# Performance work log

Hardware: AMD Instinct MI355X
Metric: run time of the kernel (lower is better)

## Reference

```python
import jax, jax.numpy as jnp
import numpy as np

B_, S_, D_, N_, R_ = 2, 2048, 1024, 16, 64  # batch, seq, d_model, d_state, dt_rank


def setup_inputs() -> dict:
    key = jax.random.key(0)
    ks = jax.random.split(key, 12)
    x = jax.random.normal(ks[0], (B_, S_, D_), dtype=jnp.float32)
    # params (xavier-ish scale)
    W_dtw = jax.random.normal(ks[1], (R_, D_), dtype=jnp.float32) * (1.0 / np.sqrt(D_))
    W_dt = jax.random.normal(ks[2], (D_, R_), dtype=jnp.float32) * (1.0 / np.sqrt(R_))
    b_dt = jnp.zeros((D_,), dtype=jnp.float32)
    A_log = jnp.log(jax.random.uniform(ks[3], (D_, N_), minval=0.5, maxval=1.5, dtype=jnp.float32))
    W_B = jax.random.normal(ks[4], (N_, D_), dtype=jnp.float32) * (1.0 / np.sqrt(D_))
    W_C = jax.random.normal(ks[5], (N_, D_), dtype=jnp.float32) * (1.0 / np.sqrt(D_))
    Dp = jnp.ones((D_,), dtype=jnp.float32)
    ln_g = jnp.ones((D_,), dtype=jnp.float32)
    ln_b = jnp.zeros((D_,), dtype=jnp.float32)
    W_out = jax.random.normal(ks[6], (D_, D_), dtype=jnp.float32) * (1.0 / np.sqrt(D_))
    return {"x": x, "W_dtw": W_dtw, "W_dt": W_dt, "b_dt": b_dt, "A_log": A_log,
            "W_B": W_B, "W_C": W_C, "Dp": Dp, "ln_g": ln_g, "ln_b": ln_b, "W_out": W_out}


def _layernorm(y, g, b, eps=1e-5):
    mu = jnp.mean(y, axis=-1, keepdims=True)
    var = jnp.mean(jnp.square(y - mu), axis=-1, keepdims=True)
    return (y - mu) * jax.lax.rsqrt(var + eps) * g + b


def reference(x, W_dtw, W_dt, b_dt, A_log, W_B, W_C, Dp, ln_g, ln_b, W_out):
    # projections
    dt = jnp.einsum('bsd,rd->bsr', x, W_dtw)                 # [B,S,R]
    delta = jax.nn.softplus(jnp.einsum('bsr,dr->bsd', dt, W_dt) + b_dt)  # [B,S,D]
    Bm = jnp.einsum('bsd,nd->bsn', x, W_B)                   # [B,S,N]
    Cm = jnp.einsum('bsd,nd->bsn', x, W_C)                   # [B,S,N]
    A = -jnp.exp(A_log)                                      # [D,N]

    def step(h, inp):
        d_t, b_t, c_t, x_t = inp                             # [B,D],[B,N],[B,N],[B,D]
        dA = jnp.exp(d_t[..., None] * A)                     # [B,D,N]
        h = dA * h + (d_t[..., None] * b_t[:, None, :]) * x_t[..., None]
        y_t = jnp.sum(h * c_t[:, None, :], axis=-1)          # [B,D]
        return h, y_t

    h0 = jnp.zeros((x.shape[0], x.shape[2], A.shape[1]), dtype=x.dtype)
    xs = (jnp.swapaxes(delta, 0, 1), jnp.swapaxes(Bm, 0, 1),
          jnp.swapaxes(Cm, 0, 1), jnp.swapaxes(x, 0, 1))
    _, ys = jax.lax.scan(step, h0, xs)                       # ys: [S,B,D]
    y = jnp.swapaxes(ys, 0, 1) + Dp * x                      # [B,S,D]
    y = _layernorm(y, ln_g, ln_b)
    return jnp.einsum('bsd,ed->bse', y, W_out)
```

## Files before the change

kernel.cpp:

```cpp
#include <hip/hip_runtime.h>
#include <hip/hip_bf16.h>

#define B_ 2
#define S_ 2048
#define D_ 1024
#define N_ 16
#define R_ 64
#define NC 64
#define CL 32
#define BS_ (B_*S_)

typedef __attribute__((ext_vector_type(4))) float f32x4;
typedef __attribute__((ext_vector_type(8))) short bf16x8;
typedef __attribute__((ext_vector_type(8))) unsigned short u16x8;

__device__ __forceinline__ unsigned short f2b(float v) {
  unsigned u = __builtin_bit_cast(unsigned, v);
  unsigned r = ((u >> 16) & 1u) + 0x7FFFu;
  return (unsigned short)((u + r) >> 16);
}

__device__ __forceinline__ void gload_lds16(const void* g, void* l) {
  __builtin_amdgcn_global_load_lds(
      (const __attribute__((address_space(1))) unsigned int*)g,
      (__attribute__((address_space(3))) unsigned int*)l, 16, 0, 0);
}

__global__ __launch_bounds__(256) void k_castall(
    const float* __restrict__ x, const float* __restrict__ W_B,
    const float* __restrict__ W_C, const float* __restrict__ W_dt,
    const float* __restrict__ W_out, const float* __restrict__ W_dtw,
    unsigned short* __restrict__ xb, unsigned short* __restrict__ WBC,
    unsigned short* __restrict__ wdtb, unsigned short* __restrict__ wob,
    unsigned short* __restrict__ wdtwT) {
  int i = (blockIdx.x * 256 + threadIdx.x) * 4;
  if (i < 5341184) {
    const float* s; unsigned short* d; int off;
    if (i < 4194304)      { s = x;     d = xb;          off = 0; }
    else if (i < 4210688) { s = W_B;   d = WBC;         off = 4194304; }
    else if (i < 4227072) { s = W_C;   d = WBC + 16384; off = 4210688; }
    else if (i < 4292608) { s = W_dt;  d = wdtb;        off = 4227072; }
    else                  { s = W_out; d = wob;         off = 4292608; }
    int j = i - off;
    float4 v = *(const float4*)&s[j];
    ushort4 o;
    o.x = f2b(v.x); o.y = f2b(v.y); o.z = f2b(v.z); o.w = f2b(v.w);
    *(ushort4*)&d[j] = o;
  } else {
    int j = i - 5341184;
    int r = j >> 10, e = j & 1023;
    float4 v = *(const float4*)&W_dtw[j];
    wdtwT[(size_t)(e + 0) * 64 + r] = f2b(v.x);
    wdtwT[(size_t)(e + 1) * 64 + r] = f2b(v.y);
    wdtwT[(size_t)(e + 2) * 64 + r] = f2b(v.z);
    wdtwT[(size_t)(e + 3) * 64 + r] = f2b(v.w);
  }
}

__global__ __launch_bounds__(256) void k_weff(
    const unsigned short* __restrict__ wdtb, const unsigned short* __restrict__ wdtwT,
    unsigned short* __restrict__ weff) {
  __shared__ __align__(16) unsigned short As[128 * 64];
  __shared__ __align__(16) unsigned short Bs[128 * 64];
  const int tid = threadIdx.x;
  const int lane = tid & 63, wid = tid >> 6;
  const int wr = wid >> 1, wc = wid & 1;
  const size_t row0 = (size_t)blockIdx.x * 128;
  const size_t col0 = (size_t)blockIdx.y * 128;
  f32x4 acc[4][4] = {};
  {
    const int r = tid >> 3, s = tid & 7;
    #pragma unroll
    for (int i = 0; i < 4; ++i) {
      const int row = i * 32 + r;
      const int gs = s ^ (row & 7);
      gload_lds16(wdtb + (row0 + row) * R_ + gs * 8, As + row * 64 + s * 8);
      gload_lds16(wdtwT + (col0 + row) * R_ + gs * 8, Bs + row * 64 + s * 8);
    }
  }
  __syncthreads();
  const int r = lane & 15, kg = lane >> 4;
  #pragma unroll
  for (int ks = 0; ks < 2; ++ks) {
    bf16x8 a[4], b[4];
    #pragma unroll
    for (int m = 0; m < 4; ++m) {
      const int arow = wr * 64 + m * 16 + r;
      a[m] = *(const bf16x8*)&As[arow * 64 + (((ks << 2) | kg) ^ (arow & 7)) * 8];
    }
    #pragma unroll
    for (int n = 0; n < 4; ++n) {
      const int brow = wc * 64 + n * 16 + r;
      b[n] = *(const bf16x8*)&Bs[brow * 64 + (((ks << 2) | kg) ^ (brow & 7)) * 8];
    }
    #pragma unroll
    for (int m = 0; m < 4; ++m)
      #pragma unroll
      for (int n = 0; n < 4; ++n)
        acc[m][n] = __builtin_amdgcn_mfma_f32_16x16x32_bf16(a[m], b[n], acc[m][n], 0, 0, 0);
  }
  const int cr = lane >> 4, cc = lane & 15;
  #pragma unroll
  for (int m = 0; m < 4; ++m)
    #pragma unroll
    for (int n = 0; n < 4; ++n)
      #pragma unroll
      for (int j = 0; j < 4; ++j)
        weff[(row0 + wr * 64 + m * 16 + cr * 4 + j) * D_ + col0 + wc * 64 + n * 16 + cc]
            = f2b(acc[m][n][j]);
}

__device__ __forceinline__ void stage64x64(const unsigned short* __restrict__ g,
                                           size_t row0, int k0,
                                           unsigned short* lds, int tid) {
  const int r = tid >> 3, s = tid & 7;
  #pragma unroll
  for (int i = 0; i < 2; ++i) {
    const int row = i * 32 + r;
    const int gs = s ^ (row & 7);
    gload_lds16(g + ((row0 + row) << 10) + k0 + (gs << 3), lds + row * 64 + s * 8);
  }
}

__global__ __launch_bounds__(256, 4) void k_deltaBC(
    const unsigned short* __restrict__ xb, const unsigned short* __restrict__ weff,
    const unsigned short* __restrict__ WBC, const float* __restrict__ b_dt,
    float* __restrict__ delta, float* __restrict__ Bm, float* __restrict__ Cm) {
  __shared__ __align__(16) unsigned short As[2][64 * 64];
  __shared__ __align__(16) unsigned short Bs[2][64 * 64];
  const int tid = threadIdx.x;
  const int lane = tid & 63, wid = tid >> 6;
  const size_t row0 = (size_t)blockIdx.x * 64;
  const int by = blockIdx.y;
  const bool bc = (by == 16);
  f32x4 acc[4] = {};

  auto stageB = [&](int buf, int k0) {
    if (!bc) {
      stage64x64(weff, (size_t)by * 64, k0, Bs[buf], tid);
    } else {
      const int row = tid >> 3, s = tid & 7;
      const int gs = s ^ (row & 7);
      gload_lds16(WBC + (size_t)row * D_ + k0 + (gs << 3), Bs[buf] + row * 64 + s * 8);
    }
  };

  stage64x64(xb, row0, 0, As[0], tid);
  stageB(0, 0);
  __syncthreads();

  int cur = 0;
  const int r = lane & 15, kg = lane >> 4;
  for (int t = 0; t < 16; ++t) {
    if (t + 1 < 16) {
      stage64x64(xb, row0, (t + 1) * 64, As[cur ^ 1], tid);
      stageB(cur ^ 1, (t + 1) * 64);
    }
    if (!bc) {
      #pragma unroll
      for (int ks = 0; ks < 2; ++ks) {
        const int arow = wid * 16 + r;
        bf16x8 a = *(const bf16x8*)&As[cur][arow * 64 + (((ks << 2) | kg) ^ (arow & 7)) * 8];
        bf16x8 b0, b1, b2, b3;
        b0 = *(const bf16x8*)&Bs[cur][(0 * 16 + r) * 64 + (((ks << 2) | kg) ^ ((0 * 16 + r) & 7)) * 8];
        b1 = *(const bf16x8*)&Bs[cur][(1 * 16 + r) * 64 + (((ks << 2) | kg) ^ ((1 * 16 + r) & 7)) * 8];
        b2 = *(const bf16x8*)&Bs[cur][(2 * 16 + r) * 64 + (((ks << 2) | kg) ^ ((2 * 16 + r) & 7)) * 8];
        b3 = *(const bf16x8*)&Bs[cur][(3 * 16 + r) * 64 + (((ks << 2) | kg) ^ ((3 * 16 + r) & 7)) * 8];
        acc[0] = __builtin_amdgcn_mfma_f32_16x16x32_bf16(a, b0, acc[0], 0, 0, 0);
        acc[1] = __builtin_amdgcn_mfma_f32_16x16x32_bf16(a, b1, acc[1], 0, 0, 0);
        acc[2] = __builtin_amdgcn_mfma_f32_16x16x32_bf16(a, b2, acc[2], 0, 0, 0);
        acc[3] = __builtin_amdgcn_mfma_f32_16x16x32_bf16(a, b3, acc[3], 0, 0, 0);
      }
    } else {
      #pragma unroll
      for (int ks = 0; ks < 2; ++ks) {
        const int arow = wid * 16 + r;
        bf16x8 a = *(const bf16x8*)&As[cur][arow * 64 + (((ks << 2) | kg) ^ (arow & 7)) * 8];
        bf16x8 b0, b1;
        b0 = *(const bf16x8*)&Bs[cur][(0 * 16 + r) * 64 + (((ks << 2) | kg) ^ ((0 * 16 + r) & 7)) * 8];
        b1 = *(const bf16x8*)&Bs[cur][(1 * 16 + r) * 64 + (((ks << 2) | kg) ^ ((1 * 16 + r) & 7)) * 8];
        acc[0] = __builtin_amdgcn_mfma_f32_16x16x32_bf16(a, b0, acc[0], 0, 0, 0);
        acc[1] = __builtin_amdgcn_mfma_f32_16x16x32_bf16(a, b1, acc[1], 0, 0, 0);
      }
    }
    __syncthreads();
    cur ^= 1;
  }

  const int cr = lane >> 4, cc = lane & 15;
  if (!bc) {
    #pragma unroll
    for (int n = 0; n < 4; ++n) {
      const int d = by * 64 + n * 16 + cc;
      const float bd = b_dt[d];
      #pragma unroll
      for (int j = 0; j < 4; ++j) {
        size_t trow = row0 + wid * 16 + cr * 4 + j;
        float v = acc[n][j] + bd;
        float sp = fmaxf(v, 0.f) + log1pf(__expf(-fabsf(v)));
        delta[trow * D_ + d] = sp;
      }
    }
  } else {
    #pragma unroll
    for (int n = 0; n < 2; ++n) {
      const int col = n * 16 + cc;
      #pragma unroll
      for (int j = 0; j < 4; ++j) {
        size_t trow = row0 + wid * 16 + cr * 4 + j;
        float v = acc[n][j];
        if (col < 16) Bm[trow * N_ + col] = v;
        else          Cm[trow * N_ + col - 16] = v;
      }
    }
  }
}

__global__ __launch_bounds__(256) void k_scan1(
    const float* __restrict__ x, const float* __restrict__ delta,
    const float* __restrict__ Bm, const float* __restrict__ A_log,
    float* __restrict__ sdsum, float* __restrict__ hend) {
  __shared__ __align__(16) float sd[CL][64];
  __shared__ __align__(16) float sx[CL][64];
  __shared__ __align__(16) float sB[CL][N_];
  const int tid = threadIdx.x;
  const int db = blockIdx.x & 15;
  const int c  = (blockIdx.x >> 4) & (NC - 1);
  const int b  = blockIdx.x >> 10;
  const int d0 = db * 64;
  const size_t tokbase = (size_t)(b * S_ + c * CL);

  {
    int s = tid >> 4, jf = (tid & 15) * 4;
    size_t g = (tokbase + s) * D_ + d0 + jf;
    gload_lds16(&delta[g], &sd[s][jf]);
    gload_lds16(&x[g],     &sx[s][jf]);
    gload_lds16(&delta[g + (size_t)16 * D_], &sd[s + 16][jf]);
    gload_lds16(&x[g + (size_t)16 * D_],     &sx[s + 16][jf]);
    if (tid < 128) {
      int s2 = tid >> 2, nf = (tid & 3) * 4;
      gload_lds16(&Bm[(tokbase + s2) * N_ + nf], &sB[s2][nf]);
    }
  }
  const int nq = tid & 3, dl = tid >> 2;
  const int d = d0 + dl;
  float4 av = *(const float4*)&A_log[(size_t)d * N_ + nq * 4];
  float Ad0 = -__expf(av.x), Ad1 = -__expf(av.y);
  float Ad2 = -__expf(av.z), Ad3 = -__expf(av.w);
  __syncthreads();

  float sds = 0.f;
  float h0 = 0.f, h1 = 0.f, h2 = 0.f, h3 = 0.f;
  #pragma unroll 8
  for (int s = 0; s < CL; ++s) {
    float dlt = sd[s][dl];
    float dbx = dlt * sx[s][dl];
    sds += dlt;
    float4 Bv = *(const float4*)&sB[s][nq * 4];
    float da0 = __expf(dlt * Ad0), da1 = __expf(dlt * Ad1);
    float da2 = __expf(dlt * Ad2), da3 = __expf(dlt * Ad3);
    h0 = da0 * h0 + dbx * Bv.x;
    h1 = da1 * h1 + dbx * Bv.y;
    h2 = da2 * h2 + dbx * Bv.z;
    h3 = da3 * h3 + dbx * Bv.w;
  }
  size_t o = (((size_t)(b * NC + c)) * D_ + d) * N_ + nq * 4;
  *(float4*)&hend[o] = make_float4(h0, h1, h2, h3);
  if (nq == 0) sdsum[(size_t)(b * NC + c) * D_ + d] = sds;
}

__global__ __launch_bounds__(256) void k_scan2(
    const float* __restrict__ sdsum, const float* __restrict__ hend,
    const float* __restrict__ A_log, float* __restrict__ hstart) {
  const int tid = threadIdx.x;
  const int o  = tid & 7;
  const int n  = (tid >> 3) & 15;
  const int dl = tid >> 7;
  const int d2 = blockIdx.x & 511;
  const int b  = blockIdx.x >> 9;
  const int d  = d2 * 2 + dl;
  const float Ad = -__expf(A_log[(size_t)d * N_ + n]);

  float ap8[8], he8[8];
  float A_loc = 1.f, H_loc = 0.f;
  #pragma unroll
  for (int k = 0; k < 8; ++k) {
    const int c = o * 8 + k;
    float sds = sdsum[(size_t)(b * NC + c) * D_ + d];
    float ap = __expf(Ad * sds);
    float he = hend[((size_t)(b * NC + c) * D_ + d) * N_ + n];
    ap8[k] = ap; he8[k] = he;
    A_loc *= ap;
    H_loc = ap * H_loc + he;
  }
  float h = 0.f;
  const int gb = (tid & 63) & ~7;
  #pragma unroll
  for (int j = 0; j < 7; ++j) {
    float Aj = __shfl(A_loc, gb | j, 64);
    float Hj = __shfl(H_loc, gb | j, 64);
    if (o > j) h = Aj * h + Hj;
  }
  #pragma unroll
  for (int k = 0; k < 8; ++k) {
    const int c = o * 8 + k;
    hstart[((size_t)(b * NC + c) * D_ + d) * N_ + n] = h;
    h = ap8[k] * h + he8[k];
  }
}

__global__ __launch_bounds__(256) void k_scan3(
    const float* __restrict__ x, const float* __restrict__ delta,
    const float* __restrict__ Bm, const float* __restrict__ Cm,
    const float* __restrict__ A_log, const float* __restrict__ hstart,
    const float* __restrict__ Dp, float* __restrict__ ypre) {
  __shared__ __align__(16) float sd[CL][64];
  __shared__ __align__(16) float sx[CL][64];
  __shared__ __align__(16) float sB[CL][N_];
  __shared__ __align__(16) float sC[CL][N_];
  __shared__ __align__(16) float sy[CL][64];
  const int tid = threadIdx.x;
  const int db = blockIdx.x & 15;
  const int c  = (blockIdx.x >> 4) & (NC - 1);
  const int b  = blockIdx.x >> 10;
  const int d0 = db * 64;
  const size_t tokbase = (size_t)(b * S_ + c * CL);

  {
    int s = tid >> 4, jf = (tid & 15) * 4;
    size_t g = (tokbase + s) * D_ + d0 + jf;
    gload_lds16(&delta[g], &sd[s][jf]);
    gload_lds16(&x[g],     &sx[s][jf]);
    gload_lds16(&delta[g + (size_t)16 * D_], &sd[s + 16][jf]);
    gload_lds16(&x[g + (size_t)16 * D_],     &sx[s + 16][jf]);
    if (tid < 128) {
      int s2 = tid >> 2, nf = (tid & 3) * 4;
      gload_lds16(&Bm[(tokbase + s2) * N_ + nf], &sB[s2][nf]);
      gload_lds16(&Cm[(tokbase + s2) * N_ + nf], &sC[s2][nf]);
    }
  }
  const int nq = tid & 3, dl = tid >> 2;
  const int d = d0 + dl;
  float4 av = *(const float4*)&A_log[(size_t)d * N_ + nq * 4];
  float Ad0 = -__expf(av.x), Ad1 = -__expf(av.y);
  float Ad2 = -__expf(av.z), Ad3 = -__expf(av.w);
  float h0, h1, h2, h3;
  {
    size_t o = (((size_t)(b * NC + c)) * D_ + d) * N_ + nq * 4;
    float4 v = *(const float4*)&hstart[o];
    h0 = v.x; h1 = v.y; h2 = v.z; h3 = v.w;
  }
  const float Dpd = Dp[d];
  __syncthreads();

  #pragma unroll 8
  for (int s = 0; s < CL; ++s) {
    float dlt = sd[s][dl];
    float xv  = sx[s][dl];
    float dbx = dlt * xv;
    float4 Bv = *(const float4*)&sB[s][nq * 4];
    float4 Cv = *(const float4*)&sC[s][nq * 4];
    float da0 = __expf(dlt * Ad0), da1 = __expf(dlt * Ad1);
    float da2 = __expf(dlt * Ad2), da3 = __expf(dlt * Ad3);
    h0 = da0 * h0 + dbx * Bv.x;
    h1 = da1 * h1 + dbx * Bv.y;
    h2 = da2 * h2 + dbx * Bv.z;
    h3 = da3 * h3 + dbx * Bv.w;
    float y = h0 * Cv.x + h1 * Cv.y + h2 * Cv.z + h3 * Cv.w;
    y += __shfl_xor(y, 1);
    y += __shfl_xor(y, 2);
    if (nq == 0) sy[s][dl] = y + Dpd * xv;
  }
  __syncthreads();
  {
    int s = tid >> 3, j = (tid & 7) * 8;
    size_t g = (tokbase + s) * D_ + d0 + j;
    *(float4*)&ypre[g]     = *(float4*)&sy[s][j];
    *(float4*)&ypre[g + 4] = *(float4*)&sy[s][j + 4];
  }
}

__device__ __forceinline__ float block_sum256(float v, float* sm) {
  #pragma unroll
  for (int o = 32; o > 0; o >>= 1) v += __shfl_down(v, o, 64);
  int w = threadIdx.x >> 6;
  __syncthreads();
  if ((threadIdx.x & 63) == 0) sm[w] = v;
  __syncthreads();
  return (sm[0] + sm[1]) + (sm[2] + sm[3]);
}

__global__ __launch_bounds__(256) void k_ln(
    const float* __restrict__ ypre, const float* __restrict__ g,
    const float* __restrict__ bta, unsigned short* __restrict__ ybf) {
  __shared__ float sm[4];
  const int t = blockIdx.x;
  const int tid = threadIdx.x;
  size_t base = (size_t)t * D_ + tid * 4;
  float4 v = *(const float4*)&ypre[base];
  float s1 = block_sum256(v.x + v.y + v.z + v.w, sm);
  float mu = s1 * (1.f / D_);
  float cx = v.x - mu, cy = v.y - mu, cz = v.z - mu, cw = v.w - mu;
  float s2 = block_sum256(cx*cx + cy*cy + cz*cz + cw*cw, sm);
  float rs = rsqrtf(s2 * (1.f / D_) + 1e-5f);
  float4 gg = *(const float4*)&g[tid * 4];
  float4 bb = *(const float4*)&bta[tid * 4];
  ushort4 o;
  o.x = f2b(cx * rs * gg.x + bb.x);
  o.y = f2b(cy * rs * gg.y + bb.y);
  o.z = f2b(cz * rs * gg.z + bb.z);
  o.w = f2b(cw * rs * gg.w + bb.w);
  *(ushort4*)&ybf[base] = o;
}

__global__ __launch_bounds__(256, 4) void k_out(const unsigned short* __restrict__ Y,
                                                const unsigned short* __restrict__ W,
                                                float* __restrict__ O) {
  __shared__ __align__(16) unsigned short As[2][64 * 64];
  __shared__ __align__(16) unsigned short Bs[2][64 * 64];
  const int tid = threadIdx.x;
  const int lane = tid & 63, wid = tid >> 6;
  const size_t row0 = (size_t)blockIdx.x * 64;
  const size_t col0 = (size_t)blockIdx.y * 64;
  f32x4 acc[4] = {};

  stage64x64(Y, row0, 0, As[0], tid);
  stage64x64(W, col0, 0, Bs[0], tid);
  __syncthreads();

  int cur = 0;
  const int r = lane & 15, kg = lane >> 4;
  for (int t = 0; t < 16; ++t) {
    if (t + 1 < 16) {
      stage64x64(Y, row0, (t + 1) * 64, As[cur ^ 1], tid);
      stage64x64(W, col0, (t + 1) * 64, Bs[cur ^ 1], tid);
    }
    #pragma unroll
    for (int ks = 0; ks < 2; ++ks) {
      const int arow = wid * 16 + r;
      bf16x8 a = *(const bf16x8*)&As[cur][arow * 64 + (((ks << 2) | kg) ^ (arow & 7)) * 8];
      bf16x8 b0, b1, b2, b3;
      b0 = *(const bf16x8*)&Bs[cur][(0 * 16 + r) * 64 + (((ks << 2) | kg) ^ ((0 * 16 + r) & 7)) * 8];
      b1 = *(const bf16x8*)&Bs[cur][(1 * 16 + r) * 64 + (((ks << 2) | kg) ^ ((1 * 16 + r) & 7)) * 8];
      b2 = *(const bf16x8*)&Bs[cur][(2 * 16 + r) * 64 + (((ks << 2) | kg) ^ ((2 * 16 + r) & 7)) * 8];
      b3 = *(const bf16x8*)&Bs[cur][(3 * 16 + r) * 64 + (((ks << 2) | kg) ^ ((3 * 16 + r) & 7)) * 8];
      acc[0] = __builtin_amdgcn_mfma_f32_16x16x32_bf16(a, b0, acc[0], 0, 0, 0);
      acc[1] = __builtin_amdgcn_mfma_f32_16x16x32_bf16(a, b1, acc[1], 0, 0, 0);
      acc[2] = __builtin_amdgcn_mfma_f32_16x16x32_bf16(a, b2, acc[2], 0, 0, 0);
      acc[3] = __builtin_amdgcn_mfma_f32_16x16x32_bf16(a, b3, acc[3], 0, 0, 0);
    }
    __syncthreads();
    cur ^= 1;
  }

  const int cr = lane >> 4, cc = lane & 15;
  #pragma unroll
  for (int n = 0; n < 4; ++n) {
    size_t orow = row0 + wid * 16 + cr * 4;
    float* op = O + orow * D_ + col0 + n * 16 + cc;
    #pragma unroll
    for (int j = 0; j < 4; ++j) op[(size_t)j * D_] = acc[n][j];
  }
}

extern "C" void kernel_launch(void* const* d_in, const int* in_sizes, int n_in,
                              void* d_out, int out_size, void* d_ws, size_t ws_size,
                              hipStream_t stream) {
  const float* x     = (const float*)d_in[0];
  const float* W_dtw = (const float*)d_in[1];
  const float* W_dt  = (const float*)d_in[2];
  const float* b_dt  = (const float*)d_in[3];
  const float* A_log = (const float*)d_in[4];
  const float* W_B   = (const float*)d_in[5];
  const float* W_C   = (const float*)d_in[6];
  const float* Dp    = (const float*)d_in[7];
  const float* ln_g  = (const float*)d_in[8];
  const float* ln_b  = (const float*)d_in[9];
  const float* W_out = (const float*)d_in[10];
  float* out = (float*)d_out;

  float* ws = (float*)d_ws;
  float* delta  = ws;
  float* ypre   = delta  + (size_t)BS_ * D_;
  float* Bm     = ypre   + (size_t)BS_ * D_;
  float* Cm     = Bm     + (size_t)BS_ * N_;
  float* hend   = Cm     + (size_t)BS_ * N_;
  float* hstart = hend   + (size_t)B_ * NC * D_ * N_;
  float* sdsum  = hstart + (size_t)B_ * NC * D_ * N_;
  unsigned short* xb    = (unsigned short*)(sdsum + (size_t)B_ * NC * D_);
  unsigned short* WBC   = xb    + (size_t)BS_ * D_;
  unsigned short* wdtb  = WBC   + (size_t)32 * D_;
  unsigned short* wdtwT = wdtb  + (size_t)D_ * R_;
  unsigned short* weff  = wdtwT + (size_t)D_ * R_;
  unsigned short* wob   = weff  + (size_t)D_ * D_;
  unsigned short* ybf   = wob   + (size_t)D_ * D_;

  k_castall<<<dim3(5280), dim3(256), 0, stream>>>(x, W_B, W_C, W_dt, W_out, W_dtw,
                                                  xb, WBC, wdtb, wob, wdtwT);
  k_weff<<<dim3(8, 8), dim3(256), 0, stream>>>(wdtb, wdtwT, weff);
  k_deltaBC<<<dim3(BS_ / 64, 17), dim3(256), 0, stream>>>(xb, weff, WBC, b_dt,
                                                          delta, Bm, Cm);
  k_scan1<<<dim3(B_ * NC * (D_ / 64)), dim3(256), 0, stream>>>(x, delta, Bm, A_log,
                                                               sdsum, hend);
  k_scan2<<<dim3(B_ * (D_ / 2)), dim3(256), 0, stream>>>(sdsum, hend, A_log, hstart);
  k_scan3<<<dim3(B_ * NC * (D_ / 64)), dim3(256), 0, stream>>>(x, delta, Bm, Cm,
                                                               A_log, hstart, Dp, ypre);
  k_ln<<<dim3(BS_), dim3(256), 0, stream>>>(ypre, ln_g, ln_b, ybf);
  k_out<<<dim3(BS_ / 64, D_ / 64), dim3(256), 0, stream>>>(ybf, wob, out);
}
```

Measured before the change: 115.8 us.

## Fuse chunked scan phases into one cooperative kernel and fold weff cast

Merges the three scan kernels into a single cooperative kernel with two grid-wide syncs. Each block handles two chunks and computes the local zero-start scan output once, then adds the carry-in correction hstart·C·exp(A·cumdelta) afterwards, so delta and x are no longer reloaded in a second full scan. The separate W_dtw transpose, cast and MFMA weff kernels are replaced by a simple FP32 dot-product path inside the cast kernel, which removes one launch. In exchange it pays for grid-sync overhead, reads B and C straight from global memory instead of LDS, and requires all 1024 blocks to be co-resident.

```diff
diff --git a/kernel.cpp b/kernel.cpp
--- a/kernel.cpp
+++ b/kernel.cpp
@@ -1,5 +1,8 @@
 #include <hip/hip_runtime.h>
 #include <hip/hip_bf16.h>
+#include <hip/hip_cooperative_groups.h>
+
+namespace cg = cooperative_groups;
 
 #define B_ 2
 #define S_ 2048
@@ -26,88 +29,39 @@
       (__attribute__((address_space(3))) unsigned int*)l, 16, 0, 0);
 }
 
-__global__ __launch_bounds__(256) void k_castall(
+__global__ __launch_bounds__(256) void k_castweff(
     const float* __restrict__ x, const float* __restrict__ W_B,
-    const float* __restrict__ W_C, const float* __restrict__ W_dt,
-    const float* __restrict__ W_out, const float* __restrict__ W_dtw,
+    const float* __restrict__ W_C, const float* __restrict__ W_out,
+    const float* __restrict__ W_dt, const float* __restrict__ W_dtw,
     unsigned short* __restrict__ xb, unsigned short* __restrict__ WBC,
-    unsigned short* __restrict__ wdtb, unsigned short* __restrict__ wob,
-    unsigned short* __restrict__ wdtwT) {
-  int i = (blockIdx.x * 256 + threadIdx.x) * 4;
-  if (i < 5341184) {
-    const float* s; unsigned short* d; int off;
-    if (i < 4194304)      { s = x;     d = xb;          off = 0; }
-    else if (i < 4210688) { s = W_B;   d = WBC;         off = 4194304; }
-    else if (i < 4227072) { s = W_C;   d = WBC + 16384; off = 4210688; }
-    else if (i < 4292608) { s = W_dt;  d = wdtb;        off = 4227072; }
-    else                  { s = W_out; d = wob;         off = 4292608; }
-    int j = i - off;
+    unsigned short* __restrict__ wob, unsigned short* __restrict__ weff) {
+  const int blk = blockIdx.x, tid = threadIdx.x;
+  if (blk < 5152) {
+    const float* s; unsigned short* d; int base;
+    if (blk < 4096)      { s = x;     d = xb;          base = 0; }
+    else if (blk < 4112) { s = W_B;   d = WBC;         base = 4096; }
+    else if (blk < 4128) { s = W_C;   d = WBC + 16384; base = 4112; }
+    else                 { s = W_out; d = wob;         base = 4128; }
+    int j = (blk - base) * 1024 + tid * 4;
     float4 v = *(const float4*)&s[j];
     ushort4 o;
     o.x = f2b(v.x); o.y = f2b(v.y); o.z = f2b(v.z); o.w = f2b(v.w);
     *(ushort4*)&d[j] = o;
   } else {
-    int j = i - 5341184;
-    int r = j >> 10, e = j & 1023;
-    float4 v = *(const float4*)&W_dtw[j];
-    wdtwT[(size_t)(e + 0) * 64 + r] = f2b(v.x);
-    wdtwT[(size_t)(e + 1) * 64 + r] = f2b(v.y);
-    wdtwT[(size_t)(e + 2) * 64 + r] = f2b(v.z);
-    wdtwT[(size_t)(e + 3) * 64 + r] = f2b(v.w);
-  }
-}
-
-__global__ __launch_bounds__(256) void k_weff(
-    const unsigned short* __restrict__ wdtb, const unsigned short* __restrict__ wdtwT,
-    unsigned short* __restrict__ weff) {
-  __shared__ __align__(16) unsigned short As[128 * 64];
-  __shared__ __align__(16) unsigned short Bs[128 * 64];
-  const int tid = threadIdx.x;
-  const int lane = tid & 63, wid = tid >> 6;
-  const int wr = wid >> 1, wc = wid & 1;
-  const size_t row0 = (size_t)blockIdx.x * 128;
-  const size_t col0 = (size_t)blockIdx.y * 128;
-  f32x4 acc[4][4] = {};
-  {
-    const int r = tid >> 3, s = tid & 7;
-    #pragma unroll
-    for (int i = 0; i < 4; ++i) {
-      const int row = i * 32 + r;
-      const int gs = s ^ (row & 7);
-      gload_lds16(wdtb + (row0 + row) * R_ + gs * 8, As + row * 64 + s * 8);
-      gload_lds16(wdtwT + (col0 + row) * R_ + gs * 8, Bs + row * 64 + s * 8);
-    }
-  }
-  __syncthreads();
-  const int r = lane & 15, kg = lane >> 4;
-  #pragma unroll
-  for (int ks = 0; ks < 2; ++ks) {
-    bf16x8 a[4], b[4];
-    #pragma unroll
-    for (int m = 0; m < 4; ++m) {
-      const int arow = wr * 64 + m * 16 + r;
-      a[m] = *(const bf16x8*)&As[arow * 64 + (((ks << 2) | kg) ^ (arow & 7)) * 8];
-    }
-    #pragma unroll
-    for (int n = 0; n < 4; ++n) {
-      const int brow = wc * 64 + n * 16 + r;
-      b[n] = *(const bf16x8*)&Bs[brow * 64 + (((ks << 2) | kg) ^ (brow & 7)) * 8];
-    }
-    #pragma unroll
-    for (int m = 0; m < 4; ++m)
-      #pragma unroll
-      for (int n = 0; n < 4; ++n)
-        acc[m][n] = __builtin_amdgcn_mfma_f32_16x16x32_bf16(a[m], b[n], acc[m][n], 0, 0, 0);
-  }
-  const int cr = lane >> 4, cc = lane & 15;
-  #pragma unroll
-  for (int m = 0; m < 4; ++m)
-    #pragma unroll
-    for (int n = 0; n < 4; ++n)
-      #pragma unroll
-      for (int j = 0; j < 4; ++j)
-        weff[(row0 + wr * 64 + m * 16 + cr * 4 + j) * D_ + col0 + wc * 64 + n * 16 + cc]
-            = f2b(acc[m][n][j]);
+    const int dd = blk - 5152;
+    const float* wdt = W_dt + (size_t)dd * R_;
+    const int e4 = tid * 4;
+    float a0 = 0.f, a1 = 0.f, a2 = 0.f, a3 = 0.f;
+    #pragma unroll 8
+    for (int r = 0; r < R_; ++r) {
+      float w = wdt[r];
+      float4 ww = *(const float4*)&W_dtw[(size_t)r * D_ + e4];
+      a0 += w * ww.x; a1 += w * ww.y; a2 += w * ww.z; a3 += w * ww.w;
+    }
+    ushort4 o;
+    o.x = f2b(a0); o.y = f2b(a1); o.z = f2b(a2); o.w = f2b(a3);
+    *(ushort4*)&weff[(size_t)dd * D_ + e4] = o;
+  }
 }
 
 __device__ __forceinline__ void stage64x64(const unsigned short* __restrict__ g,
@@ -216,30 +170,31 @@
   }
 }
 
-__global__ __launch_bounds__(256) void k_scan1(
+__global__ __launch_bounds__(256, 4) void k_scanall(
     const float* __restrict__ x, const float* __restrict__ delta,
-    const float* __restrict__ Bm, const float* __restrict__ A_log,
-    float* __restrict__ sdsum, float* __restrict__ hend) {
-  __shared__ __align__(16) float sd[CL][64];
-  __shared__ __align__(16) float sx[CL][64];
-  __shared__ __align__(16) float sB[CL][N_];
+    const float* __restrict__ Bm, const float* __restrict__ Cm,
+    const float* __restrict__ A_log, const float* __restrict__ Dp,
+    float* __restrict__ sdsum, float* __restrict__ hend,
+    float* __restrict__ hstart, float* __restrict__ ypre) {
+  __shared__ __align__(16) float sd[2][CL][64];
+  __shared__ __align__(16) float sx[2][CL][64];
   const int tid = threadIdx.x;
-  const int db = blockIdx.x & 15;
-  const int c  = (blockIdx.x >> 4) & (NC - 1);
-  const int b  = blockIdx.x >> 10;
-  const int d0 = db * 64;
-  const size_t tokbase = (size_t)(b * S_ + c * CL);
+  const int slab = blockIdx.x & 15;
+  const int cp   = (blockIdx.x >> 4) & 31;
+  const int b    = blockIdx.x >> 9;
+  const int d0 = slab * 64;
+  const int c0 = cp * 2;
 
   {
     int s = tid >> 4, jf = (tid & 15) * 4;
-    size_t g = (tokbase + s) * D_ + d0 + jf;
-    gload_lds16(&delta[g], &sd[s][jf]);
-    gload_lds16(&x[g],     &sx[s][jf]);
-    gload_lds16(&delta[g + (size_t)16 * D_], &sd[s + 16][jf]);
-    gload_lds16(&x[g + (size_t)16 * D_],     &sx[s + 16][jf]);
-    if (tid < 128) {
-      int s2 = tid >> 2, nf = (tid & 3) * 4;
-      gload_lds16(&Bm[(tokbase + s2) * N_ + nf], &sB[s2][nf]);
+    #pragma unroll
+    for (int cc = 0; cc < 2; ++cc) {
+      size_t tokb = (size_t)(b * S_ + (c0 + cc) * CL);
+      size_t g = (tokb + s) * D_ + d0 + jf;
+      gload_lds16(&delta[g],                   &sd[cc][s][jf]);
+      gload_lds16(&delta[g + (size_t)16 * D_], &sd[cc][s + 16][jf]);
+      gload_lds16(&x[g],                       &sx[cc][s][jf]);
+      gload_lds16(&x[g + (size_t)16 * D_],     &sx[cc][s + 16][jf]);
     }
   }
   const int nq = tid & 3, dl = tid >> 2;
@@ -247,136 +202,106 @@
   float4 av = *(const float4*)&A_log[(size_t)d * N_ + nq * 4];
   float Ad0 = -__expf(av.x), Ad1 = -__expf(av.y);
   float Ad2 = -__expf(av.z), Ad3 = -__expf(av.w);
-  __syncthreads();
-
-  float sds = 0.f;
-  float h0 = 0.f, h1 = 0.f, h2 = 0.f, h3 = 0.f;
-  #pragma unroll 8
-  for (int s = 0; s < CL; ++s) {
-    float dlt = sd[s][dl];
-    float dbx = dlt * sx[s][dl];
-    sds += dlt;
-    float4 Bv = *(const float4*)&sB[s][nq * 4];
-    float da0 = __expf(dlt * Ad0), da1 = __expf(dlt * Ad1);
-    float da2 = __expf(dlt * Ad2), da3 = __expf(dlt * Ad3);
-    h0 = da0 * h0 + dbx * Bv.x;
-    h1 = da1 * h1 + dbx * Bv.y;
-    h2 = da2 * h2 + dbx * Bv.z;
-    h3 = da3 * h3 + dbx * Bv.w;
-  }
-  size_t o = (((size_t)(b * NC + c)) * D_ + d) * N_ + nq * 4;
-  *(float4*)&hend[o] = make_float4(h0, h1, h2, h3);
-  if (nq == 0) sdsum[(size_t)(b * NC + c) * D_ + d] = sds;
-}
-
-__global__ __launch_bounds__(256) void k_scan2(
-    const float* __restrict__ sdsum, const float* __restrict__ hend,
-    const float* __restrict__ A_log, float* __restrict__ hstart) {
-  const int tid = threadIdx.x;
-  const int o  = tid & 7;
-  const int n  = (tid >> 3) & 15;
-  const int dl = tid >> 7;
-  const int d2 = blockIdx.x & 511;
-  const int b  = blockIdx.x >> 9;
-  const int d  = d2 * 2 + dl;
-  const float Ad = -__expf(A_log[(size_t)d * N_ + n]);
-
-  float ap8[8], he8[8];
-  float A_loc = 1.f, H_loc = 0.f;
+  const float Dpd = Dp[d];
+  __syncthreads();
+
   #pragma unroll
-  for (int k = 0; k < 8; ++k) {
-    const int c = o * 8 + k;
-    float sds = sdsum[(size_t)(b * NC + c) * D_ + d];
-    float ap = __expf(Ad * sds);
-    float he = hend[((size_t)(b * NC + c) * D_ + d) * N_ + n];
-    ap8[k] = ap; he8[k] = he;
-    A_loc *= ap;
-    H_loc = ap * H_loc + he;
-  }
-  float h = 0.f;
-  const int gb = (tid & 63) & ~7;
+  for (int cc = 0; cc < 2; ++cc) {
+    const int c = c0 + cc;
+    size_t bcb = (size_t)(b * S_ + c * CL) * N_ + nq * 4;
+    float sds = 0.f, h0 = 0.f, h1 = 0.f, h2 = 0.f, h3 = 0.f;
+    #pragma unroll 8
+    for (int s = 0; s < CL; ++s) {
+      float dlt = sd[cc][s][dl];
+      float xv  = sx[cc][s][dl];
+      float dbx = dlt * xv;
+      sds += dlt;
+      float4 Bv = *(const float4*)&Bm[bcb + (size_t)s * N_];
+      float4 Cv = *(const float4*)&Cm[bcb + (size_t)s * N_];
+      float da0 = __expf(dlt * Ad0), da1 = __expf(dlt * Ad1);
+      float da2 = __expf(dlt * Ad2), da3 = __expf(dlt * Ad3);
+      h0 = da0 * h0 + dbx * Bv.x;
+      h1 = da1 * h1 + dbx * Bv.y;
+      h2 = da2 * h2 + dbx * Bv.z;
+      h3 = da3 * h3 + dbx * Bv.w;
+      float y = h0 * Cv.x + h1 * Cv.y + h2 * Cv.z + h3 * Cv.w;
+      y += __shfl_xor(y, 1);
+      y += __shfl_xor(y, 2);
+      if (nq == 0) sx[cc][s][dl] = y + Dpd * xv;
+    }
+    size_t o = (((size_t)(b * NC + c)) * D_ + d) * N_ + nq * 4;
+    *(float4*)&hend[o] = make_float4(h0, h1, h2, h3);
+    if (nq == 0) sdsum[(size_t)(b * NC + c) * D_ + d] = sds;
+  }
+
+  cg::this_grid().sync();
+
+  {
+    const int o2  = tid & 7;
+    const int n2  = (tid >> 3) & 15;
+    const int dl2 = tid >> 7;
+    const int d22 = blockIdx.x & 511;
+    const int b2  = blockIdx.x >> 9;
+    const int dd  = d22 * 2 + dl2;
+    const float Ad = -__expf(A_log[(size_t)dd * N_ + n2]);
+    float ap8[8], he8[8];
+    float A_loc = 1.f, H_loc = 0.f;
+    #pragma unroll
+    for (int k = 0; k < 8; ++k) {
+      const int c = o2 * 8 + k;
+      float sds = sdsum[(size_t)(b2 * NC + c) * D_ + dd];
+      float ap = __expf(Ad * sds);
+      float he = hend[((size_t)(b2 * NC + c) * D_ + dd) * N_ + n2];
+      ap8[k] = ap; he8[k] = he;
+      A_loc *= ap;
+      H_loc = ap * H_loc + he;
+    }
+    float h = 0.f;
+    const int gb = (tid & 63) & ~7;
+    #pragma unroll
+    for (int j = 0; j < 7; ++j) {
+      float Aj = __shfl(A_loc, gb | j, 64);
+      float Hj = __shfl(H_loc, gb | j, 64);
+      if (o2 > j) h = Aj * h + Hj;
+    }
+    #pragma unroll
+    for (int k = 0; k < 8; ++k) {
+      const int c = o2 * 8 + k;
+      hstart[((size_t)(b2 * NC + c) * D_ + dd) * N_ + n2] = h;
+      h = ap8[k] * h + he8[k];
+    }
+  }
+
+  cg::this_grid().sync();
+
   #pragma unroll
-  for (int j = 0; j < 7; ++j) {
-    float Aj = __shfl(A_loc, gb | j, 64);
-    float Hj = __shfl(H_loc, gb | j, 64);
-    if (o > j) h = Aj * h + Hj;
-  }
-  #pragma unroll
-  for (int k = 0; k < 8; ++k) {
-    const int c = o * 8 + k;
-    hstart[((size_t)(b * NC + c) * D_ + d) * N_ + n] = h;
-    h = ap8[k] * h + he8[k];
-  }
-}
-
-__global__ __launch_bounds__(256) void k_scan3(
-    const float* __restrict__ x, const float* __restrict__ delta,
-    const float* __restrict__ Bm, const float* __restrict__ Cm,
-    const float* __restrict__ A_log, const float* __restrict__ hstart,
-    const float* __restrict__ Dp, float* __restrict__ ypre) {
-  __shared__ __align__(16) float sd[CL][64];
-  __shared__ __align__(16) float sx[CL][64];
-  __shared__ __align__(16) float sB[CL][N_];
-  __shared__ __align__(16) float sC[CL][N_];
-  __shared__ __align__(16) float sy[CL][64];
-  const int tid = threadIdx.x;
-  const int db = blockIdx.x & 15;
-  const int c  = (blockIdx.x >> 4) & (NC - 1);
-  const int b  = blockIdx.x >> 10;
-  const int d0 = db * 64;
-  const size_t tokbase = (size_t)(b * S_ + c * CL);
-
-  {
-    int s = tid >> 4, jf = (tid & 15) * 4;
-    size_t g = (tokbase + s) * D_ + d0 + jf;
-    gload_lds16(&delta[g], &sd[s][jf]);
-    gload_lds16(&x[g],     &sx[s][jf]);
-    gload_lds16(&delta[g + (size_t)16 * D_], &sd[s + 16][jf]);
-    gload_lds16(&x[g + (size_t)16 * D_],     &sx[s + 16][jf]);
-    if (tid < 128) {
-      int s2 = tid >> 2, nf = (tid & 3) * 4;
-      gload_lds16(&Bm[(tokbase + s2) * N_ + nf], &sB[s2][nf]);
-      gload_lds16(&Cm[(tokbase + s2) * N_ + nf], &sC[s2][nf]);
-    }
-  }
-  const int nq = tid & 3, dl = tid >> 2;
-  const int d = d0 + dl;
-  float4 av = *(const float4*)&A_log[(size_t)d * N_ + nq * 4];
-  float Ad0 = -__expf(av.x), Ad1 = -__expf(av.y);
-  float Ad2 = -__expf(av.z), Ad3 = -__expf(av.w);
-  float h0, h1, h2, h3;
-  {
-    size_t o = (((size_t)(b * NC + c)) * D_ + d) * N_ + nq * 4;
-    float4 v = *(const float4*)&hstart[o];
-    h0 = v.x; h1 = v.y; h2 = v.z; h3 = v.w;
-  }
-  const float Dpd = Dp[d];
-  __syncthreads();
-
-  #pragma unroll 8
-  for (int s = 0; s < CL; ++s) {
-    float dlt = sd[s][dl];
-    float xv  = sx[s][dl];
-    float dbx = dlt * xv;
-    float4 Bv = *(const float4*)&sB[s][nq * 4];
-    float4 Cv = *(const float4*)&sC[s][nq * 4];
-    float da0 = __expf(dlt * Ad0), da1 = __expf(dlt * Ad1);
-    float da2 = __expf(dlt * Ad2), da3 = __expf(dlt * Ad3);
-    h0 = da0 * h0 + dbx * Bv.x;
-    h1 = da1 * h1 + dbx * Bv.y;
-    h2 = da2 * h2 + dbx * Bv.z;
-    h3 = da3 * h3 + dbx * Bv.w;
-    float y = h0 * Cv.x + h1 * Cv.y + h2 * Cv.z + h3 * Cv.w;
-    y += __shfl_xor(y, 1);
-    y += __shfl_xor(y, 2);
-    if (nq == 0) sy[s][dl] = y + Dpd * xv;
+  for (int cc = 0; cc < 2; ++cc) {
+    const int c = c0 + cc;
+    size_t bcb = (size_t)(b * S_ + c * CL) * N_ + nq * 4;
+    float4 hs = *(const float4*)&hstart[(((size_t)(b * NC + c)) * D_ + d) * N_ + nq * 4];
+    float cum = 0.f;
+    #pragma unroll 8
+    for (int s = 0; s < CL; ++s) {
+      cum += sd[cc][s][dl];
+      float4 Cv = *(const float4*)&Cm[bcb + (size_t)s * N_];
+      float corr = hs.x * Cv.x * __expf(Ad0 * cum)
+                 + hs.y * Cv.y * __expf(Ad1 * cum)
+                 + hs.z * Cv.z * __expf(Ad2 * cum)
+                 + hs.w * Cv.w * __expf(Ad3 * cum);
+      corr += __shfl_xor(corr, 1);
+      corr += __shfl_xor(corr, 2);
+      if (nq == 0) sx[cc][s][dl] += corr;
+    }
   }
   __syncthreads();
   {
     int s = tid >> 3, j = (tid & 7) * 8;
-    size_t g = (tokbase + s) * D_ + d0 + j;
-    *(float4*)&ypre[g]     = *(float4*)&sy[s][j];
-    *(float4*)&ypre[g + 4] = *(float4*)&sy[s][j + 4];
+    #pragma unroll
+    for (int cc = 0; cc < 2; ++cc) {
+      size_t g = ((size_t)(b * S_ + (c0 + cc) * CL) + s) * D_ + d0 + j;
+      *(float4*)&ypre[g]     = *(float4*)&sx[cc][s][j];
+      *(float4*)&ypre[g + 4] = *(float4*)&sx[cc][s][j + 4];
+    }
   }
 }
 
@@ -487,24 +412,23 @@
   float* hend   = Cm     + (size_t)BS_ * N_;
   float* hstart = hend   + (size_t)B_ * NC * D_ * N_;
   float* sdsum  = hstart + (size_t)B_ * NC * D_ * N_;
-  unsigned short* xb    = (unsigned short*)(sdsum + (size_t)B_ * NC * D_);
-  unsigned short* WBC   = xb    + (size_t)BS_ * D_;
-  unsigned short* wdtb  = WBC   + (size_t)32 * D_;
-  unsigned short* wdtwT = wdtb  + (size_t)D_ * R_;
-  unsigned short* weff  = wdtwT + (size_t)D_ * R_;
-  unsigned short* wob   = weff  + (size_t)D_ * D_;
-  unsigned short* ybf   = wob   + (size_t)D_ * D_;
-
-  k_castall<<<dim3(5280), dim3(256), 0, stream>>>(x, W_B, W_C, W_dt, W_out, W_dtw,
-                                                  xb, WBC, wdtb, wob, wdtwT);
-  k_weff<<<dim3(8, 8), dim3(256), 0, stream>>>(wdtb, wdtwT, weff);
+  unsigned short* xb   = (unsigned short*)(sdsum + (size_t)B_ * NC * D_);
+  unsigned short* WBC  = xb   + (size_t)BS_ * D_;
+  unsigned short* weff = WBC  + (size_t)32 * D_;
+  unsigned short* wob  = weff + (size_t)D_ * D_;
+  unsigned short* ybf  = wob  + (size_t)D_ * D_;
+
+  k_castweff<<<dim3(6176), dim3(256), 0, stream>>>(x, W_B, W_C, W_out, W_dt, W_dtw,
+                                                   xb, WBC, wob, weff);
   k_deltaBC<<<dim3(BS_ / 64, 17), dim3(256), 0, stream>>>(xb, weff, WBC, b_dt,
                                                           delta, Bm, Cm);
-  k_scan1<<<dim3(B_ * NC * (D_ / 64)), dim3(256), 0, stream>>>(x, delta, Bm, A_log,
-                                                               sdsum, hend);
-  k_scan2<<<dim3(B_ * (D_ / 2)), dim3(256), 0, stream>>>(sdsum, hend, A_log, hstart);
-  k_scan3<<<dim3(B_ * NC * (D_ / 64)), dim3(256), 0, stream>>>(x, delta, Bm, Cm,
-                                                               A_log, hstart, Dp, ypre);
+  {
+    void* args[] = {(void*)&x, (void*)&delta, (void*)&Bm, (void*)&Cm,
+                    (void*)&A_log, (void*)&Dp, (void*)&sdsum, (void*)&hend,
+                    (void*)&hstart, (void*)&ypre};
+    hipLaunchCooperativeKernel((void*)k_scanall, dim3(B_ * (NC / 2) * 16),
+                               dim3(256), args, 0, stream);
+  }
   k_ln<<<dim3(BS_), dim3(256), 0, stream>>>(ypre, ln_g, ln_b, ybf);
   k_out<<<dim3(BS_ / 64, D_ / 64), dim3(256), 0, stream>>>(ybf, wob, out);
 }
```

Measured after the change: 387.0 us. 3.34x slower.
